# Kernel optimization log

Measured on AMD Instinct MI355X. Metric: run time of the kernel, lower is better.

Reference implementation:

```python
import jax, jax.numpy as jnp
import numpy as np

B, T, D, K = 16, 2048, 256, 4096

def setup_inputs() -> dict:
    key = jax.random.key(0)
    k1, k2 = jax.random.split(key)
    embedding_tokens = jax.random.normal(k1, (B, T, D), dtype=jnp.float32)
    # uniform(-1/K, 1/K) as in the torch init
    embeddings = jax.random.uniform(k2, (K, D), dtype=jnp.float32, minval=-1.0 / K, maxval=1.0 / K)
    return {"embedding_tokens": embedding_tokens, "embeddings": embeddings}

def reference(embedding_tokens, embeddings):
    commitment_cost = 0.5
    b, t, d = embedding_tokens.shape
    flat = embedding_tokens.reshape(-1, d)  # [N, D]
    # squared euclidean distances (same argmin as torch.cdist)
    d2 = (jnp.sum(flat * flat, axis=1, keepdims=True)
          - 2.0 * (flat @ embeddings.T)
          + jnp.sum(embeddings * embeddings, axis=1))  # [N, K]
    encoding_index = jnp.argmin(d2, axis=1)  # [N]
    quantized = embeddings[encoding_index].reshape(b, t, d)
    e_latent_loss = jnp.mean((jax.lax.stop_gradient(quantized) - embedding_tokens) ** 2)
    c_loss = commitment_cost * e_latent_loss
    # straight-through estimator
    quantized = embedding_tokens + jax.lax.stop_gradient(quantized - embedding_tokens)
    return c_loss, quantized, encoding_index.reshape(b, t)
```

## Files before the change

### kernel.cpp

```cpp
#include <hip/hip_runtime.h>

#define N_TOK 32768
#define DIM   256
#define KCB   4096
#define MROWS 64
#define XSP   260
#define NTILE (KCB / 16)
#define TILE_B 8448
#define KT    256
#define NKT   (KCB / KT)
#define DC    8
#define NDC   (DIM / DC)
#define ESD   258

#define WS_A 16
#define WS_C (16 + 4 * N_TOK)
#define WS_E (WS_C + 4 * KCB)
#define WS_NEED_NEW ((size_t)WS_E + (size_t)NTILE * TILE_B)

#define CAP    48
#define MARGIN 1.5e-3f

typedef __attribute__((ext_vector_type(8))) short short8v;
typedef __attribute__((ext_vector_type(4))) float f32x4;

__device__ __forceinline__ unsigned short f2bf_rne(float f) {
    unsigned u = __float_as_uint(f);
    unsigned r = (u + 0x7FFFu + ((u >> 16) & 1u)) >> 16;
    return (unsigned short)r;
}

__device__ __forceinline__ void gld16(const void* g, void* l) {
    __builtin_amdgcn_global_load_lds(
        (const __attribute__((address_space(1))) unsigned int*)g,
        (__attribute__((address_space(3))) unsigned int*)l, 16, 0, 0);
}
__device__ __forceinline__ void gld4(const void* g, void* l) {
    __builtin_amdgcn_global_load_lds(
        (const __attribute__((address_space(1))) unsigned int*)g,
        (__attribute__((address_space(3))) unsigned int*)l, 4, 0, 0);
}

__global__ __launch_bounds__(256) void xsq_np_kernel(const float* __restrict__ x,
                                                     float* __restrict__ A) {
#pragma clang fp contract(off)
    __shared__ float xr[4][256];
    const int tid = threadIdx.x;
    const int w = tid >> 6, l = tid & 63;
    const int row = blockIdx.x * 4 + w;
    float4 v = *(const float4*)(x + (size_t)row * DIM + l * 4);
    xr[w][l * 4 + 0] = v.x; xr[w][l * 4 + 1] = v.y;
    xr[w][l * 4 + 2] = v.z; xr[w][l * 4 + 3] = v.w;
    __syncthreads();
    const float* t = xr[w];
    const int g = (l >> 4) & 1;
    const int j = l & 15;
    const int base = g * 128 + j;
    float t0 = t[base +   0] * t[base +   0];
    float t1 = t[base +  16] * t[base +  16];
    float t2 = t[base +  32] * t[base +  32];
    float t3 = t[base +  48] * t[base +  48];
    float t4 = t[base +  64] * t[base +  64];
    float t5 = t[base +  80] * t[base +  80];
    float t6 = t[base +  96] * t[base +  96];
    float t7 = t[base + 112] * t[base + 112];
    float p = ((t0 + t1) + (t2 + t3)) + ((t4 + t5) + (t6 + t7));
    p = p + __shfl_xor(p, 8, 64);
    p = p + __shfl_xor(p, 4, 64);
    p = p + __shfl_xor(p, 2, 64);
    p = p + __shfl_xor(p, 1, 64);
    float other = __shfl(p, 16, 64);
    if (l == 0) A[row] = p + other;
}

__global__ void esq_np_kernel(const float* __restrict__ emb, float* __restrict__ C,
                              unsigned char* __restrict__ etiles) {
#pragma clang fp contract(off)
    int row  = blockIdx.x * 4 + (threadIdx.x >> 6);
    int lane = threadIdx.x & 63;
    float4 v = *(const float4*)(emb + (size_t)row * DIM + lane * 4);
    int tile = row >> 4, jj = row & 15;
    if (etiles) {
        ushort4 h;
        h.x = f2bf_rne(v.x); h.y = f2bf_rne(v.y);
        h.z = f2bf_rne(v.z); h.w = f2bf_rne(v.w);
        int f  = ((jj >> 1) & 3) | ((jj & 1) << 2);
        int u  = jj * 32 + (lane >> 1);
        int qs = u ^ f;
        *(ushort4*)(etiles + (size_t)tile * TILE_B + qs * 16 + (lane & 1) * 8) = h;
    }
    float s0 = v.x * v.x, s1 = v.y * v.y, s2 = v.z * v.z, s3 = v.w * v.w;
    double qd = (double)s0 + (double)s1 + (double)s2 + (double)s3;
    #pragma unroll
    for (int off = 32; off; off >>= 1) qd += __shfl_xor(qd, off, 64);
    if (lane == 0) {
        float cf = (float)qd;
        C[row] = cf;
        if (etiles)
            *(float*)(etiles + (size_t)tile * TILE_B + 8192 + jj * 4) = cf;
    }
}

__device__ __forceinline__ unsigned long long exact_pack(
    const float* __restrict__ emb, const float* __restrict__ C,
    const float* __restrict__ xsrow, float rowA, int k)
{
    const float4* er = (const float4*)(emb + (size_t)k * DIM);
    float acc = 0.f;
    #pragma unroll 8
    for (int d4 = 0; d4 < DIM / 4; ++d4) {
        float4 ev = er[d4];
        float4 xv = *(const float4*)(xsrow + d4 * 4);
        acc = fmaf(xv.x, ev.x, acc);
        acc = fmaf(xv.y, ev.y, acc);
        acc = fmaf(xv.z, ev.z, acc);
        acc = fmaf(xv.w, ev.w, acc);
    }
    float tmp = rowA - 2.0f * acc;
    float sc  = tmp + C[k];
    return ((unsigned long long)__float_as_uint(sc) << 32) | (unsigned)k;
}

__device__ __forceinline__ unsigned long long exact_pack2(
    const float* __restrict__ emb, const float* __restrict__ C,
    const float* __restrict__ xsrow, float rowA, int k1, int k2)
{
    const float4* e1 = (const float4*)(emb + (size_t)k1 * DIM);
    const float4* e2 = (const float4*)(emb + (size_t)k2 * DIM);
    float a1 = 0.f, a2 = 0.f;
    #pragma unroll 8
    for (int d4 = 0; d4 < DIM / 4; ++d4) {
        float4 xv = *(const float4*)(xsrow + d4 * 4);
        float4 v1 = e1[d4];
        float4 v2 = e2[d4];
        a1 = fmaf(xv.x, v1.x, a1);  a2 = fmaf(xv.x, v2.x, a2);
        a1 = fmaf(xv.y, v1.y, a1);  a2 = fmaf(xv.y, v2.y, a2);
        a1 = fmaf(xv.z, v1.z, a1);  a2 = fmaf(xv.z, v2.z, a2);
        a1 = fmaf(xv.w, v1.w, a1);  a2 = fmaf(xv.w, v2.w, a2);
    }
    float s1 = (rowA - 2.0f * a1) + C[k1];
    float s2 = (rowA - 2.0f * a2) + C[k2];
    unsigned long long p1 = ((unsigned long long)__float_as_uint(s1) << 32) | (unsigned)k1;
    unsigned long long p2 = ((unsigned long long)__float_as_uint(s2) << 32) | (unsigned)k2;
    return p1 < p2 ? p1 : p2;
}

__global__ __launch_bounds__(256, 2) void vq_mfma(
    const float* __restrict__ x, const float* __restrict__ emb,
    const unsigned char* __restrict__ etiles,
    const float* __restrict__ A, const float* __restrict__ C,
    float* __restrict__ out, double* __restrict__ lossAcc)
{
    __shared__ union {
        float xstage[MROWS][XSP];
        unsigned char ebuf[4][2][TILE_B];
        unsigned long long bestA[4][MROWS];
    } sh;
    __shared__ int    cand[MROWS][CAP];
    __shared__ int    cnt[MROWS];
    __shared__ float  thrRow[MROWS];
    __shared__ int    sIdx[MROWS];
    __shared__ double sRed[4];

    const int tid = threadIdx.x;
    const int w   = tid >> 6;
    const int l   = tid & 63;
    const int jj  = l & 15;
    const int g   = l >> 4;
    const int rowBase = blockIdx.x * MROWS;

    #pragma unroll
    for (int p = 0; p < 16; ++p) {
        int flat = p * 256 + tid;
        int row = flat >> 6, d = (flat & 63) * 4;
        *(float4*)&sh.xstage[row][d] = *(const float4*)(x + (size_t)(rowBase + row) * DIM + d);
    }
    if (tid < MROWS) { cnt[tid] = 0; thrRow[tid] = 3.4e38f; }
    __syncthreads();

    short8v Af[4][8];
    #pragma unroll
    for (int t = 0; t < 4; ++t)
        #pragma unroll
        for (int s = 0; s < 8; ++s) {
            const float* xp = &sh.xstage[t * 16 + jj][s * 32 + g * 8];
            float4 a = *(const float4*)xp;
            float4 b = *(const float4*)(xp + 4);
            short8v f;
            f[0] = (short)f2bf_rne(a.x); f[1] = (short)f2bf_rne(a.y);
            f[2] = (short)f2bf_rne(a.z); f[3] = (short)f2bf_rne(a.w);
            f[4] = (short)f2bf_rne(b.x); f[5] = (short)f2bf_rne(b.y);
            f[6] = (short)f2bf_rne(b.z); f[7] = (short)f2bf_rne(b.w);
            Af[t][s] = f;
        }
    __syncthreads();

    const int fsw = ((jj >> 1) & 3) | ((jj & 1) << 2);
    int boff[8];
    #pragma unroll
    for (int s = 0; s < 8; ++s)
        boff[s] = ((jj * 32 + s * 4 + g) ^ fsw) * 16;

    unsigned char* b0 = sh.ebuf[w][0];
    unsigned char* b1 = sh.ebuf[w][1];

#define NTOF(JV) ((((JV) & 63) * 4) + w)

#define STAGE(BUF, NT)                                                        \
    {                                                                         \
        const unsigned char* src_ = etiles + (size_t)(NT) * TILE_B;           \
        _Pragma("unroll")                                                     \
        for (int j_ = 0; j_ < 8; ++j_)                                        \
            gld16(src_ + j_ * 1024 + l * 16, (BUF) + j_ * 1024);              \
        gld4(src_ + 8192 + l * 4, (BUF) + 8192);                              \
    }

#define MFMADOT(BUF, WAITN)                                                   \
        asm volatile("s_waitcnt vmcnt(" WAITN ")" ::: "memory");              \
        float CvB = 1.0f + *(const float*)((BUF) + 8192 + jj * 4);            \
        f32x4 acc0 = {0,0,0,0}, acc1 = {0,0,0,0};                             \
        f32x4 acc2 = {0,0,0,0}, acc3 = {0,0,0,0};                             \
        __builtin_amdgcn_s_setprio(1);                                        \
        _Pragma("unroll")                                                     \
        for (int s_ = 0; s_ < 8; ++s_) {                                      \
            short8v B_ = *(const short8v*)((BUF) + boff[s_]);                 \
            acc0 = __builtin_amdgcn_mfma_f32_16x16x32_bf16(Af[0][s_], B_, acc0, 0, 0, 0); \
            acc1 = __builtin_amdgcn_mfma_f32_16x16x32_bf16(Af[1][s_], B_, acc1, 0, 0, 0); \
            acc2 = __builtin_amdgcn_mfma_f32_16x16x32_bf16(Af[2][s_], B_, acc2, 0, 0, 0); \
            acc3 = __builtin_amdgcn_mfma_f32_16x16x32_bf16(Af[3][s_], B_, acc3, 0, 0, 0); \
        }                                                                     \
        __builtin_amdgcn_s_setprio(0);

#define MINC(BUF)                                                             \
    {                                                                         \
        MFMADOT(BUF, "9")                                                     \
        _Pragma("unroll")                                                     \
        for (int r_ = 0; r_ < 4; ++r_) {                                      \
            amin[0][r_] = fminf(amin[0][r_], fmaf(-2.f, acc0[r_], CvB));      \
            amin[1][r_] = fminf(amin[1][r_], fmaf(-2.f, acc1[r_], CvB));      \
            amin[2][r_] = fminf(amin[2][r_], fmaf(-2.f, acc2[r_], CvB));      \
            amin[3][r_] = fminf(amin[3][r_], fmaf(-2.f, acc3[r_], CvB));      \
        }                                                                     \
    }

#define LOADTHR                                                               \
    {                                                                         \
        _Pragma("unroll")                                                     \
        for (int t_ = 0; t_ < 4; ++t_)                                        \
            thrv[t_] = *(const f32x4*)&thrRow[t_ * 16 + g * 4];               \
    }

#define COMPUTE(BUF, NT, WAITN)                                               \
    {                                                                         \
        MFMADOT(BUF, WAITN)                                                   \
        _Pragma("unroll")                                                     \
        for (int r_ = 0; r_ < 4; ++r_) {                                      \
            acc0[r_] = fmaf(-2.f, acc0[r_], CvB);                             \
            acc1[r_] = fmaf(-2.f, acc1[r_], CvB);                             \
            acc2[r_] = fmaf(-2.f, acc2[r_], CvB);                             \
            acc3[r_] = fmaf(-2.f, acc3[r_], CvB);                             \
        }                                                                     \
        unsigned m_ = 0;                                                      \
        _Pragma("unroll")                                                     \
        for (int r_ = 0; r_ < 4; ++r_) {                                      \
            m_ |= (acc0[r_] <= thrv[0][r_]) ? (1u << (0 + r_))  : 0u;         \
            m_ |= (acc1[r_] <= thrv[1][r_]) ? (1u << (4 + r_))  : 0u;         \
            m_ |= (acc2[r_] <= thrv[2][r_]) ? (1u << (8 + r_))  : 0u;         \
            m_ |= (acc3[r_] <= thrv[3][r_]) ? (1u << (12 + r_)) : 0u;         \
        }                                                                     \
        if (m_) {                                                             \
            int kc_ = (NT) * 16 + jj;                                         \
            do {                                                              \
                int i_ = __builtin_ctz(m_);                                   \
                m_ &= m_ - 1;                                                 \
                f32x4 va_ = (i_ & 8) ? ((i_ & 4) ? acc3 : acc2)               \
                                     : ((i_ & 4) ? acc1 : acc0);              \
                float sc_ = (i_ & 2) ? ((i_ & 1) ? va_[3] : va_[2])           \
                                     : ((i_ & 1) ? va_[1] : va_[0]);          \
                int row_ = ((i_ >> 2) << 4) + g * 4 + (i_ & 3);               \
                int p_ = atomicAdd(&cnt[row_], 1);                            \
                if (p_ < CAP) cand[row_][p_] = kc_;                           \
                if (sc_ + MARGIN < thrRow[row_])                              \
                    atomicMin((unsigned int*)&thrRow[row_],                   \
                              __float_as_uint(sc_ + MARGIN));                 \
            } while (m_);                                                     \
        }                                                                     \
    }

    float amin[4][4];
    #pragma unroll
    for (int t = 0; t < 4; ++t)
        #pragma unroll
        for (int r = 0; r < 4; ++r) amin[t][r] = 3.4e38f;

    STAGE(b0, NTOF(0));
    STAGE(b1, NTOF(1));
    #pragma unroll 1
    for (int ja = 0; ja < 8; ja += 2) {
        MINC(b0)
        STAGE(b0, NTOF(ja + 2));
        MINC(b1)
        STAGE(b1, NTOF(ja + 3));
    }

    #pragma unroll
    for (int t = 0; t < 4; ++t)
        #pragma unroll
        for (int r = 0; r < 4; ++r) {
            float v = amin[t][r];
            #pragma unroll
            for (int off = 1; off <= 8; off <<= 1)
                v = fminf(v, __shfl_xor(v, off, 16));
            if (jj == 0)
                atomicMin((unsigned int*)&thrRow[t * 16 + g * 4 + r],
                          __float_as_uint(v + MARGIN));
        }
    __syncthreads();

    f32x4 thrv[4];
    LOADTHR
    #pragma unroll 1
    for (int jv = 8; jv < 70; jv += 2) {
        COMPUTE(b0, NTOF(jv), "9");
        STAGE(b0, NTOF(jv + 2));
        COMPUTE(b1, NTOF(jv + 1), "9");
        STAGE(b1, NTOF(jv + 3));
        LOADTHR
    }
    COMPUTE(b0, NTOF(70), "9");
    COMPUTE(b1, NTOF(71), "0");
    __syncthreads();

#undef NTOF
#undef STAGE
#undef MFMADOT
#undef MINC
#undef LOADTHR
#undef COMPUTE

    const int crow = tid & 63;
    const int sub  = tid >> 6;
    unsigned long long best = ~0ULL;
    {
        int cc = cnt[crow];
        float rowA = A[rowBase + crow];
        const float* xsrow = x + (size_t)(rowBase + crow) * DIM;
        if (cc <= CAP) {
            int c = sub;
            for (; c + 4 < cc; c += 8) {
                unsigned long long pk = exact_pack2(emb, C, xsrow, rowA,
                                                   cand[crow][c], cand[crow][c + 4]);
                best = best < pk ? best : pk;
            }
            if (c < cc) {
                unsigned long long pk = exact_pack(emb, C, xsrow, rowA, cand[crow][c]);
                best = best < pk ? best : pk;
            }
        } else {
            for (int k = sub; k < KCB; k += 8) {
                unsigned long long pk = exact_pack2(emb, C, xsrow, rowA, k, k + 4);
                best = best < pk ? best : pk;
            }
        }
    }
    sh.bestA[sub][crow] = best;
    __syncthreads();
    if (tid < MROWS) {
        unsigned long long v0 = sh.bestA[0][tid], v1 = sh.bestA[1][tid];
        unsigned long long v2 = sh.bestA[2][tid], v3 = sh.bestA[3][tid];
        unsigned long long b = v0 < v1 ? v0 : v1;
        unsigned long long c2 = v2 < v3 ? v2 : v3;
        b = b < c2 ? b : c2;
        int idx = (int)(unsigned)(b & 0xFFFFFFFFull);
        sIdx[tid] = idx;
        out[1 + (size_t)N_TOK * DIM + rowBase + tid] = (float)idx;
    }
    __syncthreads();

    double lsum = 0.0;
    for (int row = 0; row < MROWS; ++row) {
        int idx = sIdx[row];
        float q  = emb[(size_t)idx * DIM + tid];
        float xv = x[(size_t)(rowBase + row) * DIM + tid];
        out[1 + (size_t)(rowBase + row) * DIM + tid] = q;
        double df = (double)q - (double)xv;
        lsum += df * df;
    }
    #pragma unroll
    for (int off = 1; off < 64; off <<= 1) lsum += __shfl_xor(lsum, off, 64);
    __syncthreads();
    if ((tid & 63) == 0) sRed[tid >> 6] = lsum;
    __syncthreads();
    if (tid == 0) atomicAdd(lossAcc, sRed[0] + sRed[1] + sRed[2] + sRed[3]);
}

__global__ __launch_bounds__(256, 2) void vq_np(
    const float* __restrict__ x, const float* __restrict__ emb,
    const float* __restrict__ A, const float* __restrict__ C,
    float* __restrict__ out, double* __restrict__ lossAcc)
{
    __shared__ float xs[MROWS][DIM];
    __shared__ float est[DC][ESD];
    __shared__ float sA[MROWS];
    __shared__ int   sIdx[MROWS];
    __shared__ double sRed[4];

    const int tid = threadIdx.x;
    const int c = tid & 31;
    const int r = tid >> 5;
    const int rowBase = blockIdx.x * MROWS;

    if (tid < MROWS) sA[tid] = A[rowBase + tid];

    #pragma unroll
    for (int p = 0; p < 16; ++p) {
        int flat = p * 256 + tid;
        int row = flat >> 6, d = (flat & 63) * 4;
        float4 v = *(const float4*)(x + (size_t)(rowBase + row) * DIM + d);
        *(float4*)&xs[row][d] = v;
    }

    float m1[8];
    int   i1[8];
    #pragma unroll
    for (int ri = 0; ri < 8; ++ri) { m1[ri] = 3.4e38f; i1[ri] = 0; }

    for (int kt = 0; kt < NKT; ++kt) {
        float acc[8][8];
        #pragma unroll
        for (int ri = 0; ri < 8; ++ri)
            #pragma unroll
            for (int kk = 0; kk < 8; ++kk) acc[ri][kk] = 0.f;

        for (int dc = 0; dc < NDC; ++dc) {
            const float* src = emb + (size_t)(kt * KT + tid) * DIM + dc * DC;
            float4 ea = *(const float4*)(src);
            float4 eb = *(const float4*)(src + 4);
            __syncthreads();
            est[0][tid] = ea.x; est[1][tid] = ea.y; est[2][tid] = ea.z; est[3][tid] = ea.w;
            est[4][tid] = eb.x; est[5][tid] = eb.y; est[6][tid] = eb.z; est[7][tid] = eb.w;
            __syncthreads();
            #pragma unroll
            for (int d4 = 0; d4 < 2; ++d4) {
                float4 xf[8];
                #pragma unroll
                for (int ri = 0; ri < 8; ++ri)
                    xf[ri] = *(const float4*)&xs[r * 8 + ri][dc * DC + d4 * 4];
                #pragma unroll
                for (int dd = 0; dd < 4; ++dd) {
                    float2 ev[4];
                    #pragma unroll
                    for (int j = 0; j < 4; ++j)
                        ev[j] = *(const float2*)&est[d4 * 4 + dd][2 * c + 64 * j];
                    #pragma unroll
                    for (int ri = 0; ri < 8; ++ri) {
                        float xv = (dd == 0) ? xf[ri].x : (dd == 1) ? xf[ri].y
                                 : (dd == 2) ? xf[ri].z : xf[ri].w;
                        #pragma unroll
                        for (int j = 0; j < 4; ++j) {
                            acc[ri][2 * j]     = fmaf(xv, ev[j].x, acc[ri][2 * j]);
                            acc[ri][2 * j + 1] = fmaf(xv, ev[j].y, acc[ri][2 * j + 1]);
                        }
                    }
                }
            }
        }
        #pragma unroll
        for (int j = 0; j < 4; ++j) {
            float2 Cv = *(const float2*)&C[kt * KT + 2 * c + 64 * j];
            #pragma unroll
            for (int p = 0; p < 2; ++p) {
                int kg = kt * KT + 2 * c + 64 * j + p;
                float Ck = (p == 0) ? Cv.x : Cv.y;
                #pragma unroll
                for (int ri = 0; ri < 8; ++ri) {
                    float tmp = sA[r * 8 + ri] - 2.0f * acc[ri][2 * j + p];
                    float s   = tmp + Ck;
                    if (s < m1[ri]) { m1[ri] = s; i1[ri] = kg; }
                }
            }
        }
    }

    #pragma unroll
    for (int ri = 0; ri < 8; ++ri) {
        float a = m1[ri]; int ja = i1[ri];
        #pragma unroll
        for (int off = 1; off <= 16; off <<= 1) {
            float b  = __shfl_xor(a, off, 64);
            int   jb = __shfl_xor(ja, off, 64);
            if (b < a || (b == a && jb < ja)) { a = b; ja = jb; }
        }
        if (c == 0) sIdx[r * 8 + ri] = ja;
    }
    __syncthreads();

    if (tid < MROWS) {
        out[1 + (size_t)N_TOK * DIM + rowBase + tid] = (float)sIdx[tid];
    }
    double lsum = 0.0;
    for (int row = 0; row < MROWS; ++row) {
        int idx = sIdx[row];
        float q  = emb[(size_t)idx * DIM + tid];
        float xv = xs[row][tid];
        out[1 + (size_t)(rowBase + row) * DIM + tid] = q;
        double df = (double)q - (double)xv;
        lsum += df * df;
    }
    #pragma unroll
    for (int off = 1; off < 64; off <<= 1) lsum += __shfl_xor(lsum, off, 64);
    __syncthreads();
    if ((tid & 63) == 0) sRed[tid >> 6] = lsum;
    __syncthreads();
    if (tid == 0) {
        atomicAdd(lossAcc, sRed[0] + sRed[1] + sRed[2] + sRed[3]);
    }
}

__global__ void finalize_kernel(const double* __restrict__ lossAcc, float* __restrict__ out) {
    out[0] = (float)(0.5 * (*lossAcc) / (double)((size_t)N_TOK * DIM));
}

extern "C" void kernel_launch(void* const* d_in, const int* in_sizes, int n_in,
                              void* d_out, int out_size, void* d_ws, size_t ws_size,
                              hipStream_t stream) {
    const float* x   = (const float*)d_in[0];
    const float* emb = (const float*)d_in[1];
    float* out = (float*)d_out;

    double* lossAcc = (double*)d_ws;
    float*  A       = (float*)((char*)d_ws + WS_A);
    float*  C       = (float*)((char*)d_ws + WS_C);
    unsigned char* etiles = (unsigned char*)((char*)d_ws + WS_E);

    const bool use_new = ws_size >= WS_NEED_NEW;

    hipMemsetAsync(d_ws, 0, 16, stream);
    xsq_np_kernel<<<N_TOK / 4, 256, 0, stream>>>(x, A);
    esq_np_kernel<<<KCB / 4, 256, 0, stream>>>(emb, C, use_new ? etiles : nullptr);
    if (use_new)
        vq_mfma<<<N_TOK / MROWS, 256, 0, stream>>>(x, emb, etiles, A, C, out, lossAcc);
    else
        vq_np<<<N_TOK / MROWS, 256, 0, stream>>>(x, emb, A, C, out, lossAcc);
    finalize_kernel<<<1, 1, 0, stream>>>(lossAcc, out);
}
```

Measured before the change: 258.4 us.

## Fuse row-norm into VQ kernel, split MFMA waits, defer candidate collection

Computes each token row's squared norm inside the main MFMA kernel from the already-staged shared-memory tile, which removes the separate xsq kernel launch and its full read of x. The MFMA dot loop is split into two halves with separate vmcnt waits, so the first half can start before the whole tile has arrived. Candidate collection (atomics on count and threshold) now runs after the next tile's prefetch is issued instead of before it, so the atomics overlap the loads. The threshold atomicMin is now unconditional, which may add LDS atomic traffic.

```diff
diff --git a/kernel.cpp b/kernel.cpp
--- a/kernel.cpp
+++ b/kernel.cpp
@@ -148,7 +148,7 @@
 __global__ __launch_bounds__(256, 2) void vq_mfma(
     const float* __restrict__ x, const float* __restrict__ emb,
     const unsigned char* __restrict__ etiles,
-    const float* __restrict__ A, const float* __restrict__ C,
+    const float* __restrict__ C,
     float* __restrict__ out, double* __restrict__ lossAcc)
 {
     __shared__ union {
@@ -159,6 +159,7 @@
     __shared__ int    cand[MROWS][CAP];
     __shared__ int    cnt[MROWS];
     __shared__ float  thrRow[MROWS];
+    __shared__ float  sA[MROWS];
     __shared__ int    sIdx[MROWS];
     __shared__ double sRed[4];
 
@@ -177,6 +178,33 @@
     }
     if (tid < MROWS) { cnt[tid] = 0; thrRow[tid] = 3.4e38f; }
     __syncthreads();
+
+    {
+#pragma clang fp contract(off)
+        const int gg = (l >> 4) & 1;
+        const int jx = l & 15;
+        const int base = gg * 128 + jx;
+        #pragma unroll 1
+        for (int rr = 0; rr < 16; ++rr) {
+            const int row = w * 16 + rr;
+            const float* t = &sh.xstage[row][0];
+            float t0 = t[base +   0] * t[base +   0];
+            float t1 = t[base +  16] * t[base +  16];
+            float t2 = t[base +  32] * t[base +  32];
+            float t3 = t[base +  48] * t[base +  48];
+            float t4 = t[base +  64] * t[base +  64];
+            float t5 = t[base +  80] * t[base +  80];
+            float t6 = t[base +  96] * t[base +  96];
+            float t7 = t[base + 112] * t[base + 112];
+            float p = ((t0 + t1) + (t2 + t3)) + ((t4 + t5) + (t6 + t7));
+            p = p + __shfl_xor(p, 8, 64);
+            p = p + __shfl_xor(p, 4, 64);
+            p = p + __shfl_xor(p, 2, 64);
+            p = p + __shfl_xor(p, 1, 64);
+            float other = __shfl(p, 16, 64);
+            if (l == 0) sA[row] = p + other;
+        }
+    }
 
     short8v Af[4][8];
     #pragma unroll
@@ -204,6 +232,12 @@
     unsigned char* b0 = sh.ebuf[w][0];
     unsigned char* b1 = sh.ebuf[w][1];
 
+    f32x4 acc0, acc1, acc2, acc3;
+    float CvB;
+    unsigned mRes;
+    int kcRes;
+    f32x4 thrv[4];
+
 #define NTOF(JV) ((((JV) & 63) * 4) + w)
 
 #define STAGE(BUF, NT)                                                        \
@@ -215,25 +249,34 @@
         gld4(src_ + 8192 + l * 4, (BUF) + 8192);                              \
     }
 
-#define MFMADOT(BUF, WAITN)                                                   \
-        asm volatile("s_waitcnt vmcnt(" WAITN ")" ::: "memory");              \
-        float CvB = 1.0f + *(const float*)((BUF) + 8192 + jj * 4);            \
-        f32x4 acc0 = {0,0,0,0}, acc1 = {0,0,0,0};                             \
-        f32x4 acc2 = {0,0,0,0}, acc3 = {0,0,0,0};                             \
+#define MFMACORE(BUF, W1, W2)                                                 \
+        asm volatile("s_waitcnt vmcnt(" W1 ")" ::: "memory");                 \
+        acc0 = (f32x4){0,0,0,0}; acc1 = (f32x4){0,0,0,0};                     \
+        acc2 = (f32x4){0,0,0,0}; acc3 = (f32x4){0,0,0,0};                     \
         __builtin_amdgcn_s_setprio(1);                                        \
         _Pragma("unroll")                                                     \
-        for (int s_ = 0; s_ < 8; ++s_) {                                      \
+        for (int s_ = 0; s_ < 4; ++s_) {                                      \
             short8v B_ = *(const short8v*)((BUF) + boff[s_]);                 \
             acc0 = __builtin_amdgcn_mfma_f32_16x16x32_bf16(Af[0][s_], B_, acc0, 0, 0, 0); \
             acc1 = __builtin_amdgcn_mfma_f32_16x16x32_bf16(Af[1][s_], B_, acc1, 0, 0, 0); \
             acc2 = __builtin_amdgcn_mfma_f32_16x16x32_bf16(Af[2][s_], B_, acc2, 0, 0, 0); \
             acc3 = __builtin_amdgcn_mfma_f32_16x16x32_bf16(Af[3][s_], B_, acc3, 0, 0, 0); \
         }                                                                     \
-        __builtin_amdgcn_s_setprio(0);
+        asm volatile("s_waitcnt vmcnt(" W2 ")" ::: "memory");                 \
+        _Pragma("unroll")                                                     \
+        for (int s_ = 4; s_ < 8; ++s_) {                                      \
+            short8v B_ = *(const short8v*)((BUF) + boff[s_]);                 \
+            acc0 = __builtin_amdgcn_mfma_f32_16x16x32_bf16(Af[0][s_], B_, acc0, 0, 0, 0); \
+            acc1 = __builtin_amdgcn_mfma_f32_16x16x32_bf16(Af[1][s_], B_, acc1, 0, 0, 0); \
+            acc2 = __builtin_amdgcn_mfma_f32_16x16x32_bf16(Af[2][s_], B_, acc2, 0, 0, 0); \
+            acc3 = __builtin_amdgcn_mfma_f32_16x16x32_bf16(Af[3][s_], B_, acc3, 0, 0, 0); \
+        }                                                                     \
+        __builtin_amdgcn_s_setprio(0);                                        \
+        CvB = 1.0f + *(const float*)((BUF) + 8192 + jj * 4);
 
 #define MINC(BUF)                                                             \
     {                                                                         \
-        MFMADOT(BUF, "9")                                                     \
+        MFMACORE(BUF, "14", "9")                                              \
         _Pragma("unroll")                                                     \
         for (int r_ = 0; r_ < 4; ++r_) {                                      \
             amin[0][r_] = fminf(amin[0][r_], fmaf(-2.f, acc0[r_], CvB));      \
@@ -250,9 +293,9 @@
             thrv[t_] = *(const f32x4*)&thrRow[t_ * 16 + g * 4];               \
     }
 
-#define COMPUTE(BUF, NT, WAITN)                                               \
+#define SCORES(BUF, NT, W1, W2)                                               \
     {                                                                         \
-        MFMADOT(BUF, WAITN)                                                   \
+        MFMACORE(BUF, W1, W2)                                                 \
         _Pragma("unroll")                                                     \
         for (int r_ = 0; r_ < 4; ++r_) {                                      \
             acc0[r_] = fmaf(-2.f, acc0[r_], CvB);                             \
@@ -260,31 +303,33 @@
             acc2[r_] = fmaf(-2.f, acc2[r_], CvB);                             \
             acc3[r_] = fmaf(-2.f, acc3[r_], CvB);                             \
         }                                                                     \
-        unsigned m_ = 0;                                                      \
+        mRes = 0;                                                             \
         _Pragma("unroll")                                                     \
         for (int r_ = 0; r_ < 4; ++r_) {                                      \
-            m_ |= (acc0[r_] <= thrv[0][r_]) ? (1u << (0 + r_))  : 0u;         \
-            m_ |= (acc1[r_] <= thrv[1][r_]) ? (1u << (4 + r_))  : 0u;         \
-            m_ |= (acc2[r_] <= thrv[2][r_]) ? (1u << (8 + r_))  : 0u;         \
-            m_ |= (acc3[r_] <= thrv[3][r_]) ? (1u << (12 + r_)) : 0u;         \
+            mRes |= (acc0[r_] <= thrv[0][r_]) ? (1u << (0 + r_))  : 0u;       \
+            mRes |= (acc1[r_] <= thrv[1][r_]) ? (1u << (4 + r_))  : 0u;       \
+            mRes |= (acc2[r_] <= thrv[2][r_]) ? (1u << (8 + r_))  : 0u;       \
+            mRes |= (acc3[r_] <= thrv[3][r_]) ? (1u << (12 + r_)) : 0u;       \
         }                                                                     \
-        if (m_) {                                                             \
-            int kc_ = (NT) * 16 + jj;                                         \
-            do {                                                              \
-                int i_ = __builtin_ctz(m_);                                   \
-                m_ &= m_ - 1;                                                 \
-                f32x4 va_ = (i_ & 8) ? ((i_ & 4) ? acc3 : acc2)               \
-                                     : ((i_ & 4) ? acc1 : acc0);              \
-                float sc_ = (i_ & 2) ? ((i_ & 1) ? va_[3] : va_[2])           \
-                                     : ((i_ & 1) ? va_[1] : va_[0]);          \
-                int row_ = ((i_ >> 2) << 4) + g * 4 + (i_ & 3);               \
-                int p_ = atomicAdd(&cnt[row_], 1);                            \
-                if (p_ < CAP) cand[row_][p_] = kc_;                           \
-                if (sc_ + MARGIN < thrRow[row_])                              \
-                    atomicMin((unsigned int*)&thrRow[row_],                   \
-                              __float_as_uint(sc_ + MARGIN));                 \
-            } while (m_);                                                     \
-        }                                                                     \
+        kcRes = (NT) * 16 + jj;                                               \
+    }
+
+#define COLLECT()                                                             \
+    if (mRes) {                                                               \
+        unsigned mm_ = mRes;                                                  \
+        do {                                                                  \
+            int i_ = __builtin_ctz(mm_);                                      \
+            mm_ &= mm_ - 1;                                                   \
+            f32x4 va_ = (i_ & 8) ? ((i_ & 4) ? acc3 : acc2)                   \
+                                 : ((i_ & 4) ? acc1 : acc0);                  \
+            float sc_ = (i_ & 2) ? ((i_ & 1) ? va_[3] : va_[2])               \
+                                 : ((i_ & 1) ? va_[1] : va_[0]);              \
+            int row_ = ((i_ >> 2) << 4) + g * 4 + (i_ & 3);                   \
+            int p_ = atomicAdd(&cnt[row_], 1);                                \
+            if (p_ < CAP) cand[row_][p_] = kcRes;                             \
+            atomicMin((unsigned int*)&thrRow[row_],                           \
+                      __float_as_uint(sc_ + MARGIN));                         \
+        } while (mm_);                                                        \
     }
 
     float amin[4][4];
@@ -317,33 +362,37 @@
         }
     __syncthreads();
 
-    f32x4 thrv[4];
     LOADTHR
     #pragma unroll 1
     for (int jv = 8; jv < 70; jv += 2) {
-        COMPUTE(b0, NTOF(jv), "9");
+        SCORES(b0, NTOF(jv), "14", "9");
         STAGE(b0, NTOF(jv + 2));
-        COMPUTE(b1, NTOF(jv + 1), "9");
+        COLLECT()
+        SCORES(b1, NTOF(jv + 1), "14", "9");
         STAGE(b1, NTOF(jv + 3));
+        COLLECT()
         LOADTHR
     }
-    COMPUTE(b0, NTOF(70), "9");
-    COMPUTE(b1, NTOF(71), "0");
+    SCORES(b0, NTOF(70), "14", "9");
+    COLLECT()
+    SCORES(b1, NTOF(71), "5", "0");
+    COLLECT()
     __syncthreads();
 
 #undef NTOF
 #undef STAGE
-#undef MFMADOT
+#undef MFMACORE
 #undef MINC
 #undef LOADTHR
-#undef COMPUTE
+#undef SCORES
+#undef COLLECT
 
     const int crow = tid & 63;
     const int sub  = tid >> 6;
     unsigned long long best = ~0ULL;
     {
         int cc = cnt[crow];
-        float rowA = A[rowBase + crow];
+        float rowA = sA[crow];
         const float* xsrow = x + (size_t)(rowBase + crow) * DIM;
         if (cc <= CAP) {
             int c = sub;
@@ -536,11 +585,13 @@
     const bool use_new = ws_size >= WS_NEED_NEW;
 
     hipMemsetAsync(d_ws, 0, 16, stream);
-    xsq_np_kernel<<<N_TOK / 4, 256, 0, stream>>>(x, A);
-    esq_np_kernel<<<KCB / 4, 256, 0, stream>>>(emb, C, use_new ? etiles : nullptr);
-    if (use_new)
-        vq_mfma<<<N_TOK / MROWS, 256, 0, stream>>>(x, emb, etiles, A, C, out, lossAcc);
-    else
+    if (use_new) {
+        esq_np_kernel<<<KCB / 4, 256, 0, stream>>>(emb, C, etiles);
+        vq_mfma<<<N_TOK / MROWS, 256, 0, stream>>>(x, emb, etiles, C, out, lossAcc);
+    } else {
+        xsq_np_kernel<<<N_TOK / 4, 256, 0, stream>>>(x, A);
+        esq_np_kernel<<<KCB / 4, 256, 0, stream>>>(emb, C, nullptr);
         vq_np<<<N_TOK / MROWS, 256, 0, stream>>>(x, emb, A, C, out, lossAcc);
+    }
     finalize_kernel<<<1, 1, 0, stream>>>(lossAcc, out);
 }
```

After: 253.2 us. 2.0% less time.
